# Optimization experiments

Measured on AMD Instinct MI355X. Metric: run time of the kernel, lower is better.

The kernel has to match this reference:

```python
import jax, jax.numpy as jnp
import numpy as np

B, S, D = 4, 2048, 512
H, Dh = 8, 64  # head_dim(=num heads)=8, qkv_dim(per-head)=64
SCALE = 1.0 / float(np.sqrt(Dh))


def setup_inputs() -> dict:
    key = jax.random.key(0)
    ks = jax.random.split(key, 11)
    w = 1.0 / float(np.sqrt(D))
    return {
        "x": jax.random.normal(ks[0], (B, S, D), dtype=jnp.float32),
        "mask": jax.random.randint(ks[1], (B, 1, S, S), 0, 2, dtype=jnp.int32),
        "Wq": jax.random.normal(ks[2], (D, H * Dh), dtype=jnp.float32) * w,
        "bq": jax.random.normal(ks[3], (H * Dh,), dtype=jnp.float32) * w,
        "Wk": jax.random.normal(ks[4], (D, H * Dh), dtype=jnp.float32) * w,
        "bk": jax.random.normal(ks[5], (H * Dh,), dtype=jnp.float32) * w,
        "Wv": jax.random.normal(ks[6], (D, H * Dh), dtype=jnp.float32) * w,
        "bv": jax.random.normal(ks[7], (H * Dh,), dtype=jnp.float32) * w,
        "Wo": jax.random.normal(ks[8], (H * Dh, D), dtype=jnp.float32) * w,
        "bo": jax.random.normal(ks[9], (D,), dtype=jnp.float32) * w,
    }


def reference(x, mask, Wq, bq, Wk, bk, Wv, bv, Wo, bo):
    b = x.shape[0]
    q = (x @ Wq + bq).reshape(b, S, H, Dh)
    k = (x @ Wk + bk).reshape(b, S, H, Dh)
    v = (x @ Wv + bv).reshape(b, S, H, Dh)
    # [b,h,q,k] attention scores, softmax over k
    score = jax.nn.softmax(jnp.einsum('bqhd,bkhd->bhqk', q, k) * SCALE, axis=-1)
    # faithful quirk: mask applied AFTER softmax, masked entries set to 1e-20
    score = jnp.where(mask == 1, jnp.float32(1e-20), score)
    # faithful quirk: einsum 'bvhd,bhqk->bvhd' sums score over q AND k -> [b,h] scalar per head
    s = score.sum(axis=(-2, -1))  # [b, h]
    att = v * s[:, None, :, None]  # [b, S, H, Dh]
    out = att.reshape(b, S, H * Dh) @ Wo + bo
    return out
```

## Files before the change

### kernel.cpp

```cpp
#include <hip/hip_runtime.h>
#include <cstdint>
#include <cstddef>

#define DEVINL __device__ __forceinline__

constexpr int S_ = 2048;
constexpr int D_ = 512;
constexpr int H_ = 8;
constexpr float SCALE_ = 0.125f;
constexpr float SCALE_L2E_ = 0.18033688011112f;

using short8 = __attribute__((ext_vector_type(8))) short;
using f32x4  = __attribute__((ext_vector_type(4))) float;

DEVINL unsigned short f2bf(float f){
  unsigned u = __builtin_bit_cast(unsigned, f);
  u += 0x7FFFu + ((u >> 16) & 1u);
  return (unsigned short)(u >> 16);
}
DEVINL float bf2f(unsigned short h){
  return __builtin_bit_cast(float, ((unsigned)h) << 16);
}

DEVINL float fast_exp2(float x){ return __builtin_amdgcn_exp2f(x); }

DEVINL void gload16(const void* g, void* l){
  __builtin_amdgcn_global_load_lds(
      (__attribute__((address_space(1))) void*)(g),
      (__attribute__((address_space(3))) void*)(l), 16, 0, 0);
}

__global__ void cast_x_kernel(const float* __restrict__ x, unsigned short* __restrict__ xb){
  int i = blockIdx.x * 256 + threadIdx.x;
  const float* p = x + (size_t)i * 8;
  float4 a = *(const float4*)p;
  float4 b = *(const float4*)(p + 4);
  short8 o;
  o[0]=f2bf(a.x); o[1]=f2bf(a.y); o[2]=f2bf(a.z); o[3]=f2bf(a.w);
  o[4]=f2bf(b.x); o[5]=f2bf(b.y); o[6]=f2bf(b.z); o[7]=f2bf(b.w);
  *(short8*)(xb + (size_t)i*8) = o;
}

__global__ void mask_bits_kernel(const int* __restrict__ mask, unsigned char* __restrict__ bits){
  unsigned tid = blockIdx.x * 256 + threadIdx.x;
  #pragma unroll
  for (int it = 0; it < 4; ++it){
    size_t bidx = (size_t)tid + (size_t)it * 524288;
    const int* p = mask + bidx * 8;
    int4 a = *(const int4*)p;
    int4 c = *(const int4*)(p + 4);
    unsigned v = (unsigned)(a.x != 0)       | ((unsigned)(a.y != 0) << 1)
               | ((unsigned)(a.z != 0) << 2) | ((unsigned)(a.w != 0) << 3)
               | ((unsigned)(c.x != 0) << 4) | ((unsigned)(c.y != 0) << 5)
               | ((unsigned)(c.z != 0) << 6) | ((unsigned)(c.w != 0) << 7);
    bits[bidx] = (unsigned char)v;
  }
}

__global__ void castT_kernel(const float* __restrict__ W0, const float* __restrict__ W1,
                             const float* __restrict__ W2, const float* __restrict__ W3,
                             unsigned short* __restrict__ WT){
  __shared__ float tile[32][33];
  const int z = blockIdx.z;
  const float* W = (z==0) ? W0 : (z==1 ? W1 : (z==2 ? W2 : W3));
  const float scale = (z==0) ? SCALE_L2E_ : 1.0f;
  unsigned short* out = WT + (size_t)z * D_ * D_;
  int n0 = blockIdx.x*32, k0 = blockIdx.y*32;
  int tx = threadIdx.x, ty = threadIdx.y;
  #pragma unroll
  for (int j=0;j<4;j++)
    tile[ty+j*8][tx] = W[(size_t)(k0+ty+j*8)*D_ + n0+tx];
  __syncthreads();
  #pragma unroll
  for (int j=0;j<4;j++)
    out[(size_t)(n0+ty+j*8)*D_ + k0+tx] = f2bf(tile[tx][ty+j*8]*scale);
}

template<typename OutT>
__global__ __launch_bounds__(256) void gemm_bt(
    const unsigned short* __restrict__ A, long long Az,
    const unsigned short* __restrict__ BT, long long Bz,
    const float* __restrict__ bias0, const float* __restrict__ bias1, const float* __restrict__ bias2,
    float bs0, float bs1, float bs2,
    OutT* __restrict__ Cp, long long Cz)
{
  __shared__ unsigned short As[128*64];
  __shared__ unsigned short Bs[128*64];
  const int z = blockIdx.z;
  const unsigned short* Ab = A + (size_t)z*Az;
  const unsigned short* Bb = BT + (size_t)z*Bz;
  const float* bias = (z==0) ? bias0 : (z==1 ? bias1 : bias2);
  const float bscale = (z==0) ? bs0 : (z==1 ? bs1 : bs2);
  OutT* C = Cp + (size_t)z*Cz;
  const int m0 = blockIdx.y*128, n0 = blockIdx.x*128;
  const int t = threadIdx.x, lane = t & 63, w = t >> 6;
  const int wr = w >> 1, wc = w & 1;
  const int g = lane >> 4, lq = lane & 15;
  f32x4 acc[4][4] = {};
  for (int kk = 0; kk < D_; kk += 64){
    #pragma unroll
    for (int p = 0; p < 4; p++){
      int o = p*4096 + t*16;
      int row = o >> 7;
      int cb  = o & 127;
      int scb = cb ^ ((row & 7) << 4);
      gload16((const char*)Ab + ((size_t)(m0+row)*D_ + kk)*2 + scb, (char*)As + o);
      gload16((const char*)Bb + ((size_t)(n0+row)*D_ + kk)*2 + scb, (char*)Bs + o);
    }
    __syncthreads();
    #pragma unroll
    for (int ks = 0; ks < 2; ks++){
      short8 af[4], bf[4];
      #pragma unroll
      for (int i = 0; i < 4; i++){
        int rowA = wr*64 + i*16 + lq;
        af[i] = *(const short8*)((const char*)As + ((rowA*128 + ks*64 + g*16) ^ ((rowA&7)<<4)));
        int rowB = wc*64 + i*16 + lq;
        bf[i] = *(const short8*)((const char*)Bs + ((rowB*128 + ks*64 + g*16) ^ ((rowB&7)<<4)));
      }
      #pragma unroll
      for (int i = 0; i < 4; i++)
        #pragma unroll
        for (int j = 0; j < 4; j++)
          acc[i][j] = __builtin_amdgcn_mfma_f32_16x16x32_bf16(af[i], bf[j], acc[i][j], 0, 0, 0);
    }
    __syncthreads();
  }
  #pragma unroll
  for (int i = 0; i < 4; i++){
    #pragma unroll
    for (int j = 0; j < 4; j++){
      int col = n0 + wc*64 + j*16 + lq;
      float bvv = bias[col]*bscale;
      #pragma unroll
      for (int r = 0; r < 4; r++){
        int row = m0 + wr*64 + i*16 + g*4 + r;
        float v = acc[i][j][r] + bvv;
        if constexpr (sizeof(OutT) == 4) C[(size_t)row*D_ + col] = (OutT)v;
        else                             C[(size_t)row*D_ + col] = (OutT)f2bf(v);
      }
    }
  }
}

__global__ __launch_bounds__(256) void attn_zm_kernel(
    const unsigned short* __restrict__ Q, const unsigned short* __restrict__ Kg,
    const unsigned* __restrict__ bitsW, float* __restrict__ Zb, float* __restrict__ Mb)
{
  __shared__ unsigned short Ks[256*64];
  const int qt = blockIdx.x, kz = blockIdx.y, zz = blockIdx.z;
  const int b = zz >> 3, h = zz & 7;
  const int t = threadIdx.x, lane = t & 63, w = t >> 6;
  const int g = lane >> 4, lq = lane & 15;
  const int qbase = qt*256 + w*64;

  const char* Kgb = (const char*)Kg + ((size_t)(b*S_ + kz*256))*1024 + h*128;
  #pragma unroll
  for (int p = 0; p < 8; p++){
    int o = p*4096 + t*16;
    int row = o >> 7;
    int cb  = o & 127;
    int scb = cb ^ ((row & 7) << 4);
    gload16(Kgb + (size_t)row*1024 + scb, (char*)Ks + o);
  }

  unsigned wb[4][8];
  #pragma unroll
  for (int qs = 0; qs < 4; qs++){
    const uint4* wp = (const uint4*)(bitsW + ((size_t)(b*S_ + qbase + qs*16 + lq))*(S_/32) + kz*8);
    uint4 wA = wp[0], wB = wp[1];
    wb[qs][0]=wA.x; wb[qs][1]=wA.y; wb[qs][2]=wA.z; wb[qs][3]=wA.w;
    wb[qs][4]=wB.x; wb[qs][5]=wB.y; wb[qs][6]=wB.z; wb[qs][7]=wB.w;
  }

  short8 qf[4][2];
  #pragma unroll
  for (int qs = 0; qs < 4; qs++)
    #pragma unroll
    for (int c = 0; c < 2; c++)
      qf[qs][c] = *(const short8*)(Q + ((size_t)(b*S_ + qbase + qs*16 + lq))*D_ + h*64 + c*32 + g*8);

  float Z[4], Mm[4];
  #pragma unroll
  for (int qs = 0; qs < 4; qs++){ Z[qs] = 0.f; Mm[qs] = 0.f; }

  __syncthreads();

  #pragma unroll
  for (int i = 0; i < 16; ++i){
    const int kt2 = i >> 1, ks = i & 1;
    const int row = i*16 + lq;
    const int sw = (row & 7) << 4;
    short8 A0 = *(const short8*)((const char*)Ks + row*128 + ((g*16) ^ sw));
    short8 A1 = *(const short8*)((const char*)Ks + row*128 + ((64 + g*16) ^ sw));
    #pragma unroll
    for (int qs = 0; qs < 4; qs++){
      f32x4 d = {0.f,0.f,0.f,0.f};
      d = __builtin_amdgcn_mfma_f32_16x16x32_bf16(A0, qf[qs][0], d, 0, 0, 0);
      d = __builtin_amdgcn_mfma_f32_16x16x32_bf16(A1, qf[qs][1], d, 0, 0, 0);
      unsigned nib = wb[qs][kt2] >> (ks*16 + g*4);
      #pragma unroll
      for (int r = 0; r < 4; r++){
        float p = fast_exp2(d[r]);
        Z[qs] += p;
        Mm[qs] = fmaf((float)((nib >> r) & 1u), p, Mm[qs]);
      }
    }
  }
  #pragma unroll
  for (int qs = 0; qs < 4; qs++){
    Z[qs]  += __shfl_xor(Z[qs], 16);  Mm[qs] += __shfl_xor(Mm[qs], 16);
    Z[qs]  += __shfl_xor(Z[qs], 32);  Mm[qs] += __shfl_xor(Mm[qs], 32);
  }
  if (g == 0){
    int base = (b*H_ + h)*S_ + qbase + lq;
    #pragma unroll
    for (int qs = 0; qs < 4; qs++){
      atomicAdd(&Zb[base + qs*16], Z[qs]);
      atomicAdd(&Mb[base + qs*16], Mm[qs]);
    }
  }
}

__global__ __launch_bounds__(256) void finalize_s(const float* __restrict__ Zb,
                                                  const float* __restrict__ Mb,
                                                  float* __restrict__ sbh){
  const int bh = blockIdx.x;
  const int t = threadIdx.x;
  const float* Z = Zb + (size_t)bh*S_;
  const float* M = Mb + (size_t)bh*S_;
  float acc = 0.f;
  #pragma unroll
  for (int q = t; q < S_; q += 256){
    float z = Z[q];
    acc += (z - M[q]) / z;
  }
  #pragma unroll
  for (int m = 1; m < 64; m <<= 1) acc += __shfl_xor(acc, m);
  __shared__ float wsum[4];
  if ((t & 63) == 0) wsum[t >> 6] = acc;
  __syncthreads();
  if (t == 0) sbh[bh] = wsum[0] + wsum[1] + wsum[2] + wsum[3];
}

__global__ void scale_woT_kernel(const unsigned short* __restrict__ WoT,
                                 const float* __restrict__ sbh,
                                 unsigned short* __restrict__ outw){
  int i = blockIdx.x*256 + threadIdx.x;
  size_t e = (size_t)i * 8;
  int k = (int)(e & 511);
  int n = (int)((e >> 9) & 511);
  int b = (int)(e >> 18);
  float sv = sbh[b*H_ + (k >> 6)];
  short8 wv = *(const short8*)(WoT + (size_t)n*D_ + k);
  short8 o;
  #pragma unroll
  for (int j = 0; j < 8; j++) o[j] = (short)f2bf(bf2f((unsigned short)wv[j]) * sv);
  *(short8*)(outw + e) = o;
}

extern "C" void kernel_launch(void* const* d_in, const int* in_sizes, int n_in,
                              void* d_out, int out_size, void* d_ws, size_t ws_size,
                              hipStream_t stream) {
  (void)in_sizes; (void)n_in; (void)out_size; (void)ws_size;
  const float* x  = (const float*)d_in[0];
  const int* mask = (const int*)d_in[1];
  const float* Wq = (const float*)d_in[2];
  const float* bq = (const float*)d_in[3];
  const float* Wk = (const float*)d_in[4];
  const float* bk = (const float*)d_in[5];
  const float* Wv = (const float*)d_in[6];
  const float* bv = (const float*)d_in[7];
  const float* Wo = (const float*)d_in[8];
  const float* bo = (const float*)d_in[9];
  float* out = (float*)d_out;

  char* ws = (char*)d_ws;
  unsigned short* xb   = (unsigned short*)(ws);
  unsigned short* wT   = (unsigned short*)(ws +  8388608);
  unsigned short* woT  = (unsigned short*)(ws +  9961472);
  unsigned short* Qb   = (unsigned short*)(ws + 10485760);
  unsigned short* Kb   = (unsigned short*)(ws + 18874368);
  unsigned short* Vb   = (unsigned short*)(ws + 27262976);
  unsigned short* woST = (unsigned short*)(ws + 35651584);
  float*          sbh  = (float*)         (ws + 37748736);
  float*          Zbuf = (float*)(ws);
  float*          Mbuf = (float*)(ws + 262144);
  unsigned char*  bits = (unsigned char*)(ws + 35651584);

  cast_x_kernel<<<2048, 256, 0, stream>>>(x, xb);
  castT_kernel<<<dim3(16,16,4), dim3(32,8), 0, stream>>>(Wq, Wk, Wv, Wo, wT);
  mask_bits_kernel<<<2048, 256, 0, stream>>>(mask, bits);

  gemm_bt<unsigned short><<<dim3(4,64,3), 256, 0, stream>>>(
      xb, 0LL, wT, 262144LL, bq, bk, bv, SCALE_L2E_, 1.0f, 1.0f, Qb, 4194304LL);

  hipMemsetAsync(Zbuf, 0, 524288, stream);

  attn_zm_kernel<<<dim3(8,8,32), 256, 0, stream>>>(Qb, Kb, (const unsigned*)bits, Zbuf, Mbuf);
  finalize_s<<<32, 256, 0, stream>>>(Zbuf, Mbuf, sbh);

  scale_woT_kernel<<<512, 256, 0, stream>>>(woT, sbh, woST);

  gemm_bt<float><<<dim3(4,16,4), 256, 0, stream>>>(
      Vb, 1048576LL, woST, 262144LL, bo, bo, bo, 1.0f, 1.0f, 1.0f, out, 1048576LL);
}
```

Before: 109.7 us.

## Fold V projection into output weights to skip the V GEMM

Instead of computing V = x·Wv and then (s·V)·Wo, the code precomputes a per-batch combined weight W2 = (Wo scaled by s)ᵀ·Wv with a small GEMM, plus a folded bias bo + bv·Wo_scaled. The final GEMM then multiplies x directly by W2, so the large V projection GEMM and its bf16 intermediate are removed. The attention partial sums are also accumulated as vectors, with horizontal adds per query block. The trade-off is an extra rounding to bf16 of the fused weight and a serial dependency, since the combined weight can only be built after the attention sums finish.

```diff
diff --git a/kernel.cpp b/kernel.cpp
--- a/kernel.cpp
+++ b/kernel.cpp
@@ -58,11 +58,10 @@
 }
 
 __global__ void castT_kernel(const float* __restrict__ W0, const float* __restrict__ W1,
-                             const float* __restrict__ W2, const float* __restrict__ W3,
-                             unsigned short* __restrict__ WT){
+                             const float* __restrict__ W2, unsigned short* __restrict__ WT){
   __shared__ float tile[32][33];
   const int z = blockIdx.z;
-  const float* W = (z==0) ? W0 : (z==1 ? W1 : (z==2 ? W2 : W3));
+  const float* W = (z==0) ? W0 : (z==1 ? W1 : W2);
   const float scale = (z==0) ? SCALE_L2E_ : 1.0f;
   unsigned short* out = WT + (size_t)z * D_ * D_;
   int n0 = blockIdx.x*32, k0 = blockIdx.y*32;
@@ -80,8 +79,9 @@
 __global__ __launch_bounds__(256) void gemm_bt(
     const unsigned short* __restrict__ A, long long Az,
     const unsigned short* __restrict__ BT, long long Bz,
-    const float* __restrict__ bias0, const float* __restrict__ bias1, const float* __restrict__ bias2,
-    float bs0, float bs1, float bs2,
+    const float* __restrict__ bias0, const float* __restrict__ bias1,
+    const float* __restrict__ bias2, const float* __restrict__ bias3,
+    float bs0, float bs1, float bs2, float bs3,
     OutT* __restrict__ Cp, long long Cz)
 {
   __shared__ unsigned short As[128*64];
@@ -89,8 +89,8 @@
   const int z = blockIdx.z;
   const unsigned short* Ab = A + (size_t)z*Az;
   const unsigned short* Bb = BT + (size_t)z*Bz;
-  const float* bias = (z==0) ? bias0 : (z==1 ? bias1 : bias2);
-  const float bscale = (z==0) ? bs0 : (z==1 ? bs1 : bs2);
+  const float* bias = (z==0) ? bias0 : (z==1 ? bias1 : (z==2 ? bias2 : bias3));
+  const float bscale = (z==0) ? bs0 : (z==1 ? bs1 : (z==2 ? bs2 : bs3));
   OutT* C = Cp + (size_t)z*Cz;
   const int m0 = blockIdx.y*128, n0 = blockIdx.x*128;
   const int t = threadIdx.x, lane = t & 63, w = t >> 6;
@@ -180,9 +180,12 @@
     for (int c = 0; c < 2; c++)
       qf[qs][c] = *(const short8*)(Q + ((size_t)(b*S_ + qbase + qs*16 + lq))*D_ + h*64 + c*32 + g*8);
 
-  float Z[4], Mm[4];
-  #pragma unroll
-  for (int qs = 0; qs < 4; qs++){ Z[qs] = 0.f; Mm[qs] = 0.f; }
+  f32x4 Z4[4], M4[4];
+  #pragma unroll
+  for (int qs = 0; qs < 4; qs++){
+    Z4[qs] = (f32x4){0.f,0.f,0.f,0.f};
+    M4[qs] = (f32x4){0.f,0.f,0.f,0.f};
+  }
 
   __syncthreads();
 
@@ -199,25 +202,26 @@
       d = __builtin_amdgcn_mfma_f32_16x16x32_bf16(A0, qf[qs][0], d, 0, 0, 0);
       d = __builtin_amdgcn_mfma_f32_16x16x32_bf16(A1, qf[qs][1], d, 0, 0, 0);
       unsigned nib = wb[qs][kt2] >> (ks*16 + g*4);
+      f32x4 p, mf;
       #pragma unroll
       for (int r = 0; r < 4; r++){
-        float p = fast_exp2(d[r]);
-        Z[qs] += p;
-        Mm[qs] = fmaf((float)((nib >> r) & 1u), p, Mm[qs]);
+        p[r]  = fast_exp2(d[r]);
+        mf[r] = (float)((nib >> r) & 1u);
       }
+      Z4[qs] += p;
+      M4[qs] += mf * p;
     }
   }
   #pragma unroll
   for (int qs = 0; qs < 4; qs++){
-    Z[qs]  += __shfl_xor(Z[qs], 16);  Mm[qs] += __shfl_xor(Mm[qs], 16);
-    Z[qs]  += __shfl_xor(Z[qs], 32);  Mm[qs] += __shfl_xor(Mm[qs], 32);
-  }
-  if (g == 0){
-    int base = (b*H_ + h)*S_ + qbase + lq;
-    #pragma unroll
-    for (int qs = 0; qs < 4; qs++){
-      atomicAdd(&Zb[base + qs*16], Z[qs]);
-      atomicAdd(&Mb[base + qs*16], Mm[qs]);
+    float z = (Z4[qs][0] + Z4[qs][1]) + (Z4[qs][2] + Z4[qs][3]);
+    float m = (M4[qs][0] + M4[qs][1]) + (M4[qs][2] + M4[qs][3]);
+    z += __shfl_xor(z, 16);  m += __shfl_xor(m, 16);
+    z += __shfl_xor(z, 32);  m += __shfl_xor(m, 32);
+    if (g == 0){
+      int base = (b*H_ + h)*S_ + qbase + qs*16 + lq;
+      atomicAdd(&Zb[base], z);
+      atomicAdd(&Mb[base], m);
     }
   }
 }
@@ -257,6 +261,27 @@
   #pragma unroll
   for (int j = 0; j < 8; j++) o[j] = (short)f2bf(bf2f((unsigned short)wv[j]) * sv);
   *(short8*)(outw + e) = o;
+}
+
+__global__ __launch_bounds__(256) void bo2_kernel(const unsigned short* __restrict__ woST,
+                                                  const float* __restrict__ bv,
+                                                  const float* __restrict__ bo,
+                                                  float* __restrict__ bo2){
+  const int b = blockIdx.x >> 1;
+  const int n = (blockIdx.x & 1)*256 + threadIdx.x;
+  const unsigned short* row = woST + ((size_t)b*D_ + n)*D_;
+  float acc = 0.f;
+  #pragma unroll
+  for (int c = 0; c < D_; c += 8){
+    short8 w8 = *(const short8*)(row + c);
+    float4 b0 = *(const float4*)(bv + c);
+    float4 b1 = *(const float4*)(bv + c + 4);
+    acc += bf2f((unsigned short)w8[0])*b0.x + bf2f((unsigned short)w8[1])*b0.y
+         + bf2f((unsigned short)w8[2])*b0.z + bf2f((unsigned short)w8[3])*b0.w
+         + bf2f((unsigned short)w8[4])*b1.x + bf2f((unsigned short)w8[5])*b1.y
+         + bf2f((unsigned short)w8[6])*b1.z + bf2f((unsigned short)w8[7])*b1.w;
+  }
+  bo2[b*D_ + n] = bo[n] + acc;
 }
 
 extern "C" void kernel_launch(void* const* d_in, const int* in_sizes, int n_in,
@@ -278,22 +303,25 @@
   char* ws = (char*)d_ws;
   unsigned short* xb   = (unsigned short*)(ws);
   unsigned short* wT   = (unsigned short*)(ws +  8388608);
-  unsigned short* woT  = (unsigned short*)(ws +  9961472);
+  unsigned short* woT  = (unsigned short*)(ws +  8388608 + 2*524288);
   unsigned short* Qb   = (unsigned short*)(ws + 10485760);
   unsigned short* Kb   = (unsigned short*)(ws + 18874368);
-  unsigned short* Vb   = (unsigned short*)(ws + 27262976);
+  float*          Zbuf = (float*)(ws + 27262976);
+  float*          Mbuf = (float*)(ws + 27525120);
+  unsigned short* Wvb  = (unsigned short*)(ws + 27787264);
+  unsigned short* W2T  = (unsigned short*)(ws + 28311552);
   unsigned short* woST = (unsigned short*)(ws + 35651584);
   float*          sbh  = (float*)         (ws + 37748736);
-  float*          Zbuf = (float*)(ws);
-  float*          Mbuf = (float*)(ws + 262144);
+  float*          bo2  = (float*)         (ws + 37748864);
   unsigned char*  bits = (unsigned char*)(ws + 35651584);
 
   cast_x_kernel<<<2048, 256, 0, stream>>>(x, xb);
-  castT_kernel<<<dim3(16,16,4), dim3(32,8), 0, stream>>>(Wq, Wk, Wv, Wo, wT);
+  cast_x_kernel<<<128, 256, 0, stream>>>(Wv, Wvb);
+  castT_kernel<<<dim3(16,16,3), dim3(32,8), 0, stream>>>(Wq, Wk, Wo, wT);
   mask_bits_kernel<<<2048, 256, 0, stream>>>(mask, bits);
 
-  gemm_bt<unsigned short><<<dim3(4,64,3), 256, 0, stream>>>(
-      xb, 0LL, wT, 262144LL, bq, bk, bv, SCALE_L2E_, 1.0f, 1.0f, Qb, 4194304LL);
+  gemm_bt<unsigned short><<<dim3(4,64,2), 256, 0, stream>>>(
+      xb, 0LL, wT, 262144LL, bq, bk, bk, bk, SCALE_L2E_, 1.0f, 0.f, 0.f, Qb, 4194304LL);
 
   hipMemsetAsync(Zbuf, 0, 524288, stream);
 
@@ -302,6 +330,12 @@
 
   scale_woT_kernel<<<512, 256, 0, stream>>>(woT, sbh, woST);
 
+  gemm_bt<unsigned short><<<dim3(4,4,4), 256, 0, stream>>>(
+      woST, 262144LL, Wvb, 0LL, bo, bo, bo, bo, 0.f, 0.f, 0.f, 0.f, W2T, 262144LL);
+
+  bo2_kernel<<<8, 256, 0, stream>>>(woST, bv, bo, bo2);
+
   gemm_bt<float><<<dim3(4,16,4), 256, 0, stream>>>(
-      Vb, 1048576LL, woST, 262144LL, bo, bo, bo, 1.0f, 1.0f, 1.0f, out, 1048576LL);
-}
+      xb, 1048576LL, W2T, 262144LL, bo2, bo2+512, bo2+1024, bo2+1536,
+      1.f, 1.f, 1.f, 1.f, out, 1048576LL);
+}
```

New measurement: 144.1 us. 1.31x slower.
